# Kernel tuning notes

Measured on AMD Instinct MI355X. Metric: run time of the kernel, lower is better.

The kernel has to match this reference:

```python
import jax, jax.numpy as jnp
import numpy as np

OBS_LEN = 8
PRED_LEN = 12
BATCH = 65536
EMB = 64
H = 64


def setup_inputs() -> dict:
    key = jax.random.key(0)
    ks = jax.random.split(key, 18)
    s = 1.0 / np.sqrt(H)  # torch default uniform bound scale, used as std here

    def p(k, shape):
        return (jax.random.normal(k, shape, dtype=jnp.float32) * s).astype(jnp.float32)

    return {
        "obs_traj": jax.random.normal(ks[0], (OBS_LEN, BATCH, 2), dtype=jnp.float32),
        "obs_traj_rel": jax.random.normal(ks[1], (OBS_LEN, BATCH, 2), dtype=jnp.float32),
        # encoder params
        "enc_emb_w": p(ks[2], (EMB, 2)),
        "enc_emb_b": p(ks[3], (EMB,)),
        "enc_w_ih": p(ks[4], (4 * H, EMB)),
        "enc_w_hh": p(ks[5], (4 * H, H)),
        "enc_b_ih": p(ks[6], (4 * H,)),
        "enc_b_hh": p(ks[7], (4 * H,)),
        # decoder params
        "dec_emb_w": p(ks[8], (EMB, 2)),
        "dec_emb_b": p(ks[9], (EMB,)),
        "dec_w_ih": p(ks[10], (4 * H, EMB)),
        "dec_w_hh": p(ks[11], (4 * H, H)),
        "dec_b_ih": p(ks[12], (4 * H,)),
        "dec_b_hh": p(ks[13], (4 * H,)),
        "h2p_w": p(ks[14], (2, H)),
        "h2p_b": p(ks[15], (2,)),
    }


def _lstm_cell(h, c, x, w_ih, w_hh, b_ih, b_hh):
    # torch nn.LSTM gate order: i, f, g, o
    gates = x @ w_ih.T + h @ w_hh.T + (b_ih + b_hh)
    i, f, g, o = jnp.split(gates, 4, axis=-1)
    c_new = jax.nn.sigmoid(f) * c + jax.nn.sigmoid(i) * jnp.tanh(g)
    h_new = jax.nn.sigmoid(o) * jnp.tanh(c_new)
    return h_new, c_new


def reference(obs_traj, obs_traj_rel,
              enc_emb_w, enc_emb_b, enc_w_ih, enc_w_hh, enc_b_ih, enc_b_hh,
              dec_emb_w, dec_emb_b, dec_w_ih, dec_w_hh, dec_b_ih, dec_b_hh,
              h2p_w, h2p_b):
    batch = obs_traj_rel.shape[1]

    # ---------- Encoder ----------
    enc_in = obs_traj_rel @ enc_emb_w.T + enc_emb_b  # [T, B, EMB]

    def enc_step(carry, x_t):
        h, c = carry
        h, c = _lstm_cell(h, c, x_t, enc_w_ih, enc_w_hh, enc_b_ih, enc_b_hh)
        return (h, c), None

    h0 = jnp.zeros((batch, H), dtype=obs_traj_rel.dtype)
    c0 = jnp.zeros((batch, H), dtype=obs_traj_rel.dtype)
    (h_enc, _), _ = jax.lax.scan(enc_step, (h0, c0), enc_in)

    # ---------- Decoder ----------
    dec_h = h_enc                                   # final encoder hidden seeds decoder
    dec_c = jnp.zeros((batch, H), dtype=obs_traj_rel.dtype)
    last_pos_rel = obs_traj_rel[-1]
    dec_in = last_pos_rel @ dec_emb_w.T + dec_emb_b  # [B, EMB]

    def dec_step(carry, _):
        h, c, x = carry
        h, c = _lstm_cell(h, c, x, dec_w_ih, dec_w_hh, dec_b_ih, dec_b_hh)
        rel_pos = h @ h2p_w.T + h2p_b               # [B, 2]
        x_next = rel_pos @ dec_emb_w.T + dec_emb_b  # [B, EMB]
        return (h, c, x_next), rel_pos

    (_, _, _), pred_traj_fake_rel = jax.lax.scan(
        dec_step, (dec_h, dec_c, dec_in), None, length=PRED_LEN)
    return pred_traj_fake_rel  # [PRED_LEN, B, 2]
```

## Files before the change

kernel.cpp:

```cpp
#include <hip/hip_runtime.h>

#define OBS_LEN 8
#define PRED_LEN 12
#define TILE_B 64
#define NTHREADS 256
#define HSTR 72

typedef __attribute__((ext_vector_type(8))) short short8;
typedef __attribute__((ext_vector_type(4))) float floatx4;
typedef __attribute__((ext_vector_type(2))) float floatx2;
typedef __attribute__((ext_vector_type(4))) unsigned short ushortx4;
typedef unsigned short u16;
typedef unsigned int u32;

__device__ __forceinline__ u16 f2bf(float f) {
  __bf16 b = (__bf16)f;
  return __builtin_bit_cast(u16, b);
}
__device__ __forceinline__ float bf2f(u16 h) {
  return __builtin_bit_cast(float, ((u32)h) << 16);
}
__device__ __forceinline__ float rndbf(float f) { return (float)(__bf16)f; }

#if __has_builtin(__builtin_amdgcn_exp2f)
__device__ __forceinline__ float fexp2_(float x) { return __builtin_amdgcn_exp2f(x); }
#else
__device__ __forceinline__ float fexp2_(float x) { return exp2f(x); }
#endif
#if __has_builtin(__builtin_amdgcn_rcpf)
__device__ __forceinline__ float rcp_nr(float x) {
  float r = __builtin_amdgcn_rcpf(x);
  return r * (2.0f - x * r);
}
#else
__device__ __forceinline__ float rcp_nr(float x) { return 1.0f / x; }
#endif

#define L2E 1.442695040888963f

__device__ __forceinline__ floatx4 mfma_bf(short8 a, short8 b, floatx4 c) {
  return __builtin_amdgcn_mfma_f32_16x16x32_bf16(a, b, c, 0, 0, 0);
}

__device__ __forceinline__ void load_afrags(const float* __restrict__ W,
                                            short8 (&af)[4][2],
                                            int u0, int q, int l16) {
#pragma unroll
  for (int t = 0; t < 4; ++t)
#pragma unroll
    for (int kf = 0; kf < 2; ++kf) {
      const float* src = W + (t * 64 + u0 + l16) * 64 + kf * 32 + q * 8;
      const floatx4 w0 = *(const floatx4*)src;
      const floatx4 w1 = *(const floatx4*)(src + 4);
      short8 a;
#pragma unroll
      for (int j = 0; j < 4; ++j) {
        a[j] = (short)f2bf(w0[j]);
        a[j + 4] = (short)f2bf(w1[j]);
      }
      af[t][kf] = a;
    }
}

__device__ __forceinline__ void bstep_h(const u16* __restrict__ rdh,
                                        const short8 (&afh)[4][2],
                                        const float (&bv)[4][4],
                                        floatx4 (&acc)[4][4], int q, int l16) {
#pragma unroll
  for (int n = 0; n < 4; ++n)
#pragma unroll
    for (int t = 0; t < 4; ++t)
#pragma unroll
      for (int r = 0; r < 4; ++r) acc[n][t][r] = bv[t][r];
#pragma unroll
  for (int n = 0; n < 4; ++n) {
    const int s = n * 16 + l16;
    const short8 hb0 = *(const short8*)(rdh + s * HSTR + q * 8);
    const short8 hb1 = *(const short8*)(rdh + s * HSTR + 32 + q * 8);
#pragma unroll
    for (int t = 0; t < 4; ++t) {
      acc[n][t] = mfma_bf(afh[t][0], hb0, acc[n][t]);
      acc[n][t] = mfma_bf(afh[t][1], hb1, acc[n][t]);
    }
  }
}

__device__ __forceinline__ void bstep_x(const u16* __restrict__ rdx,
                                        u16* __restrict__ wrh,
                                        const short8 (&afx)[4][2],
                                        floatx4 (&acc)[4][4], float (&c)[4][4],
                                        int q, int l16, int u0) {
#pragma unroll
  for (int n = 0; n < 4; ++n) {
    const int s = n * 16 + l16;
    const short8 xb0 = *(const short8*)(rdx + s * HSTR + q * 8);
    const short8 xb1 = *(const short8*)(rdx + s * HSTR + 32 + q * 8);
#pragma unroll
    for (int t = 0; t < 4; ++t) {
      acc[n][t] = mfma_bf(afx[t][0], xb0, acc[n][t]);
      acc[n][t] = mfma_bf(afx[t][1], xb1, acc[n][t]);
    }
  }
#pragma unroll
  for (int n = 0; n < 4; ++n) {
    const int s = n * 16 + l16;
    ushortx4 o;
#pragma unroll
    for (int r = 0; r < 4; ++r) {
      const float ig = acc[n][0][r], fg = acc[n][1][r];
      const float gg = acc[n][2][r], og = acc[n][3][r];
      const float ei = fexp2_(ig * -L2E);
      const float ef = fexp2_(fg * -L2E);
      const float eg = fexp2_(gg * (2.0f * L2E));
      const float eo = fexp2_(og * -L2E);
      const float A = 1.0f + ei;
      const float Bg = eg + 1.0f;
      const float F = 1.0f + ef;
      const float P = A * Bg;
      const float cc = (c[n][r] * P + (eg - 1.0f) * F) * rcp_nr(F * P);
      c[n][r] = cc;
      const float ec = fexp2_(cc * (2.0f * L2E));
      const float h = (ec - 1.0f) * rcp_nr((1.0f + eo) * (ec + 1.0f));
      o[r] = f2bf(h);
    }
    *(ushortx4*)(wrh + s * HSTR + u0 + q * 4) = o;
  }
}

__device__ __forceinline__ void axphase(const float* __restrict__ orow,
                                        const float* __restrict__ ew0,
                                        const float* __restrict__ ew1,
                                        const float* __restrict__ eb,
                                        u16* __restrict__ xw, int s, int p) {
  const floatx2 rr = *(const floatx2*)(orow + s * 2);
  const float r0 = rndbf(rr.x);
  const float r1 = rndbf(rr.y);
#pragma unroll
  for (int i4 = 0; i4 < 4; ++i4) {
    ushortx4 v;
#pragma unroll
    for (int ii = 0; ii < 4; ++ii) {
      const int e = p * 16 + i4 * 4 + ii;
      const float xe = r0 * ew0[e] + r1 * ew1[e] + eb[e];
      v[ii] = f2bf(xe);
    }
    *(ushortx4*)(xw + s * HSTR + p * 16 + i4 * 4) = v;
  }
}

__device__ __forceinline__ void areldot(const u16* __restrict__ h,
                                        const float* __restrict__ hw0,
                                        const float* __restrict__ hw1,
                                        float b2p0, float b2p1, int s, int p,
                                        float& r0, float& r1) {
  float d0 = 0.f, d1 = 0.f;
#pragma unroll
  for (int i4 = 0; i4 < 4; ++i4) {
    const ushortx4 hv4 = *(const ushortx4*)(h + s * HSTR + p * 16 + i4 * 4);
#pragma unroll
    for (int ii = 0; ii < 4; ++ii) {
      const int u = p * 16 + i4 * 4 + ii;
      const float hv = bf2f(hv4[ii]);
      d0 += hv * hw0[u];
      d1 += hv * hw1[u];
    }
  }
  d0 += __shfl_xor(d0, 1);
  d0 += __shfl_xor(d0, 2);
  d1 += __shfl_xor(d1, 1);
  d1 += __shfl_xor(d1, 2);
  r0 = d0 + b2p0;
  r1 = d1 + b2p1;
}

__global__ void __launch_bounds__(NTHREADS, 2)
lstm_kernel(const float* __restrict__ obs_rel,
            const float* __restrict__ enc_emb_w, const float* __restrict__ enc_emb_b,
            const float* __restrict__ enc_w_ih, const float* __restrict__ enc_w_hh,
            const float* __restrict__ enc_b_ih, const float* __restrict__ enc_b_hh,
            const float* __restrict__ dec_emb_w, const float* __restrict__ dec_emb_b,
            const float* __restrict__ dec_w_ih, const float* __restrict__ dec_w_hh,
            const float* __restrict__ dec_b_ih, const float* __restrict__ dec_b_hh,
            const float* __restrict__ h2p_w, const float* __restrict__ h2p_b,
            float* __restrict__ out, int batch) {
  __shared__ __align__(16) u16 hS[2][TILE_B * HSTR];
  __shared__ __align__(16) u16 xS[2][TILE_B * HSTR];
  __shared__ float ew0e[64], ew1e[64], ebe[64];
  __shared__ float ew0d[64], ew1d[64], ebd[64];
  __shared__ float hw0[64], hw1[64];

  const int tid = threadIdx.x;
  const int wv = tid >> 6, lane = tid & 63;
  const int q = lane >> 4, l16 = lane & 15;
  const int u0 = wv << 4;
  const int s4 = tid >> 2, p4 = tid & 3;
  const long S0 = (long)blockIdx.x * TILE_B;

  if (tid < 64) {
    ew0e[tid] = rndbf(enc_emb_w[tid * 2]);
    ew1e[tid] = rndbf(enc_emb_w[tid * 2 + 1]);
    ebe[tid] = enc_emb_b[tid];
    ew0d[tid] = rndbf(dec_emb_w[tid * 2]);
    ew1d[tid] = rndbf(dec_emb_w[tid * 2 + 1]);
    ebd[tid] = dec_emb_b[tid];
    hw0[tid] = rndbf(h2p_w[tid]);
    hw1[tid] = rndbf(h2p_w[64 + tid]);
  }
  for (int i = tid; i < TILE_B * HSTR / 2; i += NTHREADS) ((u32*)&hS[0][0])[i] = 0;

  short8 afh[4][2], afx[4][2];
  floatx4 acc[4][4];
  float bv[4][4], c[4][4];
  load_afrags(enc_w_hh, afh, u0, q, l16);
  load_afrags(enc_w_ih, afx, u0, q, l16);
#pragma unroll
  for (int t = 0; t < 4; ++t)
#pragma unroll
    for (int r = 0; r < 4; ++r) {
      const int g = t * 64 + u0 + q * 4 + r;
      bv[t][r] = enc_b_ih[g] + enc_b_hh[g];
      c[t][r] = 0.f;
    }
  const float b2p0 = h2p_b[0], b2p1 = h2p_b[1];
  __syncthreads();
  axphase(obs_rel + S0 * 2, ew0e, ew1e, ebe, xS[0], s4, p4);
  __syncthreads();

  int pb = 0;
#pragma unroll 1
  for (int t = 0; t < OBS_LEN; ++t) {
    const int tn = t + 1;
    const float* orow = obs_rel + (long)((tn < 8) ? tn : 7) * batch * 2 + S0 * 2;
    if (tn < 8)
      axphase(orow, ew0e, ew1e, ebe, xS[tn & 1], s4, p4);
    else
      axphase(orow, ew0d, ew1d, ebd, xS[0], s4, p4);
    bstep_h(hS[pb], afh, bv, acc, q, l16);
    bstep_x(xS[t & 1], hS[pb ^ 1], afx, acc, c, q, l16, u0);
    __syncthreads();
    pb ^= 1;
  }

  load_afrags(dec_w_hh, afh, u0, q, l16);
  load_afrags(dec_w_ih, afx, u0, q, l16);
#pragma unroll
  for (int t = 0; t < 4; ++t)
#pragma unroll
    for (int r = 0; r < 4; ++r) {
      const int g = t * 64 + u0 + q * 4 + r;
      bv[t][r] = dec_b_ih[g] + dec_b_hh[g];
      c[t][r] = 0.f;
    }
  bstep_h(hS[pb], afh, bv, acc, q, l16);
  bstep_x(xS[0], hS[pb ^ 1], afx, acc, c, q, l16, u0);
  __syncthreads();
  pb ^= 1;

#pragma unroll 1
  for (int j = 1; j < PRED_LEN; ++j) {
    float r0, r1;
    areldot(hS[pb], hw0, hw1, b2p0, b2p1, s4, p4, r0, r1);
    if (p4 == 0)
      *(floatx2*)(out + (long)(j - 1) * batch * 2 + (S0 + s4) * 2) = floatx2{r0, r1};
    {
      const float rb0 = rndbf(r0), rb1 = rndbf(r1);
#pragma unroll
      for (int i4 = 0; i4 < 4; ++i4) {
        ushortx4 v;
#pragma unroll
        for (int ii = 0; ii < 4; ++ii) {
          const int e = p4 * 16 + i4 * 4 + ii;
          const float xe = rb0 * ew0d[e] + rb1 * ew1d[e] + ebd[e];
          v[ii] = f2bf(xe);
        }
        *(ushortx4*)(&xS[0][0] + s4 * HSTR + p4 * 16 + i4 * 4) = v;
      }
    }
    bstep_h(hS[pb], afh, bv, acc, q, l16);
    __syncthreads();
    bstep_x(xS[0], hS[pb ^ 1], afx, acc, c, q, l16, u0);
    __syncthreads();
    pb ^= 1;
  }

  {
    float r0, r1;
    areldot(hS[pb], hw0, hw1, b2p0, b2p1, s4, p4, r0, r1);
    if (p4 == 0)
      *(floatx2*)(out + (long)(PRED_LEN - 1) * batch * 2 + (S0 + s4) * 2) =
          floatx2{r0, r1};
  }
}

extern "C" void kernel_launch(void* const* d_in, const int* in_sizes, int n_in,
                              void* d_out, int out_size, void* d_ws, size_t ws_size,
                              hipStream_t stream) {
  const float* obs_rel = (const float*)d_in[1];
  const int batch = in_sizes[1] / (OBS_LEN * 2);

  const int blocks = batch / TILE_B;
  hipLaunchKernelGGL(lstm_kernel, dim3(blocks), dim3(NTHREADS), 0, stream,
                     obs_rel,
                     (const float*)d_in[2], (const float*)d_in[3],
                     (const float*)d_in[4], (const float*)d_in[5],
                     (const float*)d_in[6], (const float*)d_in[7],
                     (const float*)d_in[8], (const float*)d_in[9],
                     (const float*)d_in[10], (const float*)d_in[11],
                     (const float*)d_in[12], (const float*)d_in[13],
                     (const float*)d_in[14], (const float*)d_in[15],
                     (float*)d_out, batch);
}
```

Measured before the change: 240.5 us.

## Fuse LSTM h/x GEMMs per batch slice to cut accumulators and raise occupancy

Merges the separate hidden and input MFMA passes into one cell step that processes each 16-row batch slice fully, so only 4 accumulators are live instead of 16. The gate math and embedding generation are rewritten with float2 vectors so the compiler can use packed FP32 ops. Launch bounds go from 2 to 3 blocks per SIMD-set. The decoder's h-MFMA no longer overlaps the barrier after the x write, which loses some latency hiding, and the tighter register budget risks spills.

```diff
diff --git a/kernel.cpp b/kernel.cpp
--- a/kernel.cpp
+++ b/kernel.cpp
@@ -10,8 +10,11 @@
 typedef __attribute__((ext_vector_type(4))) float floatx4;
 typedef __attribute__((ext_vector_type(2))) float floatx2;
 typedef __attribute__((ext_vector_type(4))) unsigned short ushortx4;
+typedef __attribute__((ext_vector_type(2))) unsigned int u32x2;
 typedef unsigned short u16;
 typedef unsigned int u32;
+
+#define L2E 1.442695040888963f
 
 __device__ __forceinline__ u16 f2bf(float f) {
   __bf16 b = (__bf16)f;
@@ -27,16 +30,24 @@
 #else
 __device__ __forceinline__ float fexp2_(float x) { return exp2f(x); }
 #endif
+__device__ __forceinline__ floatx2 exp2v(floatx2 x) {
+  floatx2 r;
+  r.x = fexp2_(x.x);
+  r.y = fexp2_(x.y);
+  return r;
+}
 #if __has_builtin(__builtin_amdgcn_rcpf)
-__device__ __forceinline__ float rcp_nr(float x) {
-  float r = __builtin_amdgcn_rcpf(x);
+__device__ __forceinline__ floatx2 rcp2(floatx2 x) {
+  floatx2 r;
+  r.x = __builtin_amdgcn_rcpf(x.x);
+  r.y = __builtin_amdgcn_rcpf(x.y);
   return r * (2.0f - x * r);
 }
 #else
-__device__ __forceinline__ float rcp_nr(float x) { return 1.0f / x; }
+__device__ __forceinline__ floatx2 rcp2(floatx2 x) {
+  return floatx2{1.0f / x.x, 1.0f / x.y};
+}
 #endif
-
-#define L2E 1.442695040888963f
 
 __device__ __forceinline__ floatx4 mfma_bf(short8 a, short8 b, floatx4 c) {
   return __builtin_amdgcn_mfma_f32_16x16x32_bf16(a, b, c, 0, 0, 0);
@@ -62,118 +73,101 @@
     }
 }
 
-__device__ __forceinline__ void bstep_h(const u16* __restrict__ rdh,
-                                        const short8 (&afh)[4][2],
-                                        const float (&bv)[4][4],
-                                        floatx4 (&acc)[4][4], int q, int l16) {
-#pragma unroll
-  for (int n = 0; n < 4; ++n)
-#pragma unroll
-    for (int t = 0; t < 4; ++t)
-#pragma unroll
-      for (int r = 0; r < 4; ++r) acc[n][t][r] = bv[t][r];
+__device__ __forceinline__ void cell_step(const u16* __restrict__ rdh,
+                                          const u16* __restrict__ rdx,
+                                          u16* __restrict__ wrh,
+                                          const short8 (&afh)[4][2],
+                                          const short8 (&afx)[4][2],
+                                          const floatx4 (&bacc)[4],
+                                          floatx2 (&c)[4][2],
+                                          int q, int l16, int u0) {
 #pragma unroll
   for (int n = 0; n < 4; ++n) {
     const int s = n * 16 + l16;
     const short8 hb0 = *(const short8*)(rdh + s * HSTR + q * 8);
     const short8 hb1 = *(const short8*)(rdh + s * HSTR + 32 + q * 8);
-#pragma unroll
-    for (int t = 0; t < 4; ++t) {
-      acc[n][t] = mfma_bf(afh[t][0], hb0, acc[n][t]);
-      acc[n][t] = mfma_bf(afh[t][1], hb1, acc[n][t]);
-    }
-  }
-}
-
-__device__ __forceinline__ void bstep_x(const u16* __restrict__ rdx,
-                                        u16* __restrict__ wrh,
-                                        const short8 (&afx)[4][2],
-                                        floatx4 (&acc)[4][4], float (&c)[4][4],
-                                        int q, int l16, int u0) {
-#pragma unroll
-  for (int n = 0; n < 4; ++n) {
-    const int s = n * 16 + l16;
     const short8 xb0 = *(const short8*)(rdx + s * HSTR + q * 8);
     const short8 xb1 = *(const short8*)(rdx + s * HSTR + 32 + q * 8);
-#pragma unroll
-    for (int t = 0; t < 4; ++t) {
-      acc[n][t] = mfma_bf(afx[t][0], xb0, acc[n][t]);
-      acc[n][t] = mfma_bf(afx[t][1], xb1, acc[n][t]);
-    }
-  }
-#pragma unroll
-  for (int n = 0; n < 4; ++n) {
-    const int s = n * 16 + l16;
-    ushortx4 o;
-#pragma unroll
-    for (int r = 0; r < 4; ++r) {
-      const float ig = acc[n][0][r], fg = acc[n][1][r];
-      const float gg = acc[n][2][r], og = acc[n][3][r];
-      const float ei = fexp2_(ig * -L2E);
-      const float ef = fexp2_(fg * -L2E);
-      const float eg = fexp2_(gg * (2.0f * L2E));
-      const float eo = fexp2_(og * -L2E);
-      const float A = 1.0f + ei;
-      const float Bg = eg + 1.0f;
-      const float F = 1.0f + ef;
-      const float P = A * Bg;
-      const float cc = (c[n][r] * P + (eg - 1.0f) * F) * rcp_nr(F * P);
-      c[n][r] = cc;
-      const float ec = fexp2_(cc * (2.0f * L2E));
-      const float h = (ec - 1.0f) * rcp_nr((1.0f + eo) * (ec + 1.0f));
-      o[r] = f2bf(h);
-    }
-    *(ushortx4*)(wrh + s * HSTR + u0 + q * 4) = o;
-  }
-}
-
-__device__ __forceinline__ void axphase(const float* __restrict__ orow,
-                                        const float* __restrict__ ew0,
-                                        const float* __restrict__ ew1,
-                                        const float* __restrict__ eb,
-                                        u16* __restrict__ xw, int s, int p) {
-  const floatx2 rr = *(const floatx2*)(orow + s * 2);
-  const float r0 = rndbf(rr.x);
-  const float r1 = rndbf(rr.y);
+    floatx4 acc[4];
+#pragma unroll
+    for (int t = 0; t < 4; ++t) acc[t] = mfma_bf(afh[t][0], hb0, bacc[t]);
+#pragma unroll
+    for (int t = 0; t < 4; ++t) acc[t] = mfma_bf(afx[t][0], xb0, acc[t]);
+#pragma unroll
+    for (int t = 0; t < 4; ++t) acc[t] = mfma_bf(afh[t][1], hb1, acc[t]);
+#pragma unroll
+    for (int t = 0; t < 4; ++t) acc[t] = mfma_bf(afx[t][1], xb1, acc[t]);
+    u32 hpk[2];
+#pragma unroll
+    for (int p = 0; p < 2; ++p) {
+      const floatx2 iv = {acc[0][2 * p], acc[0][2 * p + 1]};
+      const floatx2 fv = {acc[1][2 * p], acc[1][2 * p + 1]};
+      const floatx2 gv = {acc[2][2 * p], acc[2][2 * p + 1]};
+      const floatx2 ov = {acc[3][2 * p], acc[3][2 * p + 1]};
+      const floatx2 ei = exp2v(iv * -L2E);
+      const floatx2 ef = exp2v(fv * -L2E);
+      const floatx2 eg = exp2v(gv * (2.0f * L2E));
+      const floatx2 eo = exp2v(ov * -L2E);
+      const floatx2 A = ei + 1.0f;
+      const floatx2 F = ef + 1.0f;
+      const floatx2 Bg = eg + 1.0f;
+      const floatx2 P = A * Bg;
+      const floatx2 num = c[n][p] * P + (eg - 1.0f) * F;
+      const floatx2 cn = num * rcp2(F * P);
+      c[n][p] = cn;
+      const floatx2 ec = exp2v(cn * (2.0f * L2E));
+      const floatx2 h = (ec - 1.0f) * rcp2((eo + 1.0f) * (ec + 1.0f));
+      hpk[p] = (u32)f2bf(h.x) | ((u32)f2bf(h.y) << 16);
+    }
+    *(u32x2*)(wrh + s * HSTR + u0 + q * 4) = u32x2{hpk[0], hpk[1]};
+  }
+}
+
+__device__ __forceinline__ void xgen16(float rb0, float rb1,
+                                       const float* __restrict__ ew0,
+                                       const float* __restrict__ ew1,
+                                       const float* __restrict__ eb,
+                                       u16* __restrict__ xw, int s, int p) {
 #pragma unroll
   for (int i4 = 0; i4 < 4; ++i4) {
-    ushortx4 v;
-#pragma unroll
-    for (int ii = 0; ii < 4; ++ii) {
-      const int e = p * 16 + i4 * 4 + ii;
-      const float xe = r0 * ew0[e] + r1 * ew1[e] + eb[e];
-      v[ii] = f2bf(xe);
-    }
-    *(ushortx4*)(xw + s * HSTR + p * 16 + i4 * 4) = v;
+    const int e = p * 16 + i4 * 4;
+    const floatx2 wa0 = *(const floatx2*)(ew0 + e);
+    const floatx2 wa1 = *(const floatx2*)(ew0 + e + 2);
+    const floatx2 wb0 = *(const floatx2*)(ew1 + e);
+    const floatx2 wb1 = *(const floatx2*)(ew1 + e + 2);
+    const floatx2 ba0 = *(const floatx2*)(eb + e);
+    const floatx2 ba1 = *(const floatx2*)(eb + e + 2);
+    const floatx2 x0 = wa0 * rb0 + (wb0 * rb1 + ba0);
+    const floatx2 x1 = wa1 * rb0 + (wb1 * rb1 + ba1);
+    const u32x2 pk = {(u32)f2bf(x0.x) | ((u32)f2bf(x0.y) << 16),
+                      (u32)f2bf(x1.x) | ((u32)f2bf(x1.y) << 16)};
+    *(u32x2*)(xw + s * HSTR + e) = pk;
   }
 }
 
 __device__ __forceinline__ void areldot(const u16* __restrict__ h,
-                                        const float* __restrict__ hw0,
-                                        const float* __restrict__ hw1,
+                                        const floatx2* __restrict__ hwp,
                                         float b2p0, float b2p1, int s, int p,
                                         float& r0, float& r1) {
-  float d0 = 0.f, d1 = 0.f;
+  floatx2 d = {0.f, 0.f};
 #pragma unroll
   for (int i4 = 0; i4 < 4; ++i4) {
     const ushortx4 hv4 = *(const ushortx4*)(h + s * HSTR + p * 16 + i4 * 4);
 #pragma unroll
     for (int ii = 0; ii < 4; ++ii) {
       const int u = p * 16 + i4 * 4 + ii;
-      const float hv = bf2f(hv4[ii]);
-      d0 += hv * hw0[u];
-      d1 += hv * hw1[u];
-    }
-  }
-  d0 += __shfl_xor(d0, 1);
-  d0 += __shfl_xor(d0, 2);
-  d1 += __shfl_xor(d1, 1);
-  d1 += __shfl_xor(d1, 2);
-  r0 = d0 + b2p0;
-  r1 = d1 + b2p1;
-}
-
-__global__ void __launch_bounds__(NTHREADS, 2)
+      d = hwp[u] * bf2f(hv4[ii]) + d;
+    }
+  }
+  d.x += __shfl_xor(d.x, 1);
+  d.x += __shfl_xor(d.x, 2);
+  d.y += __shfl_xor(d.y, 1);
+  d.y += __shfl_xor(d.y, 2);
+  r0 = d.x + b2p0;
+  r1 = d.y + b2p1;
+}
+
+__global__ void __launch_bounds__(NTHREADS, 3)
 lstm_kernel(const float* __restrict__ obs_rel,
             const float* __restrict__ enc_emb_w, const float* __restrict__ enc_emb_b,
             const float* __restrict__ enc_w_ih, const float* __restrict__ enc_w_hh,
@@ -187,7 +181,7 @@
   __shared__ __align__(16) u16 xS[2][TILE_B * HSTR];
   __shared__ float ew0e[64], ew1e[64], ebe[64];
   __shared__ float ew0d[64], ew1d[64], ebd[64];
-  __shared__ float hw0[64], hw1[64];
+  __shared__ __align__(8) floatx2 hwp[64];
 
   const int tid = threadIdx.x;
   const int wv = tid >> 6, lane = tid & 63;
@@ -203,27 +197,31 @@
     ew0d[tid] = rndbf(dec_emb_w[tid * 2]);
     ew1d[tid] = rndbf(dec_emb_w[tid * 2 + 1]);
     ebd[tid] = dec_emb_b[tid];
-    hw0[tid] = rndbf(h2p_w[tid]);
-    hw1[tid] = rndbf(h2p_w[64 + tid]);
+    hwp[tid] = floatx2{rndbf(h2p_w[tid]), rndbf(h2p_w[64 + tid])};
   }
   for (int i = tid; i < TILE_B * HSTR / 2; i += NTHREADS) ((u32*)&hS[0][0])[i] = 0;
 
   short8 afh[4][2], afx[4][2];
-  floatx4 acc[4][4];
-  float bv[4][4], c[4][4];
+  floatx4 bacc[4];
+  floatx2 c[4][2];
   load_afrags(enc_w_hh, afh, u0, q, l16);
   load_afrags(enc_w_ih, afx, u0, q, l16);
 #pragma unroll
-  for (int t = 0; t < 4; ++t)
+  for (int t = 0; t < 4; ++t) {
 #pragma unroll
     for (int r = 0; r < 4; ++r) {
       const int g = t * 64 + u0 + q * 4 + r;
-      bv[t][r] = enc_b_ih[g] + enc_b_hh[g];
-      c[t][r] = 0.f;
-    }
+      bacc[t][r] = enc_b_ih[g] + enc_b_hh[g];
+    }
+  }
+#pragma unroll
+  for (int n = 0; n < 4; ++n) c[n][0] = c[n][1] = floatx2{0.f, 0.f};
   const float b2p0 = h2p_b[0], b2p1 = h2p_b[1];
   __syncthreads();
-  axphase(obs_rel + S0 * 2, ew0e, ew1e, ebe, xS[0], s4, p4);
+  {
+    const floatx2 rr = *(const floatx2*)(obs_rel + (S0 + s4) * 2);
+    xgen16(rndbf(rr.x), rndbf(rr.y), ew0e, ew1e, ebe, xS[0], s4, p4);
+  }
   __syncthreads();
 
   int pb = 0;
@@ -231,12 +229,12 @@
   for (int t = 0; t < OBS_LEN; ++t) {
     const int tn = t + 1;
     const float* orow = obs_rel + (long)((tn < 8) ? tn : 7) * batch * 2 + S0 * 2;
+    const floatx2 rr = *(const floatx2*)(orow + s4 * 2);
     if (tn < 8)
-      axphase(orow, ew0e, ew1e, ebe, xS[tn & 1], s4, p4);
+      xgen16(rndbf(rr.x), rndbf(rr.y), ew0e, ew1e, ebe, xS[tn & 1], s4, p4);
     else
-      axphase(orow, ew0d, ew1d, ebd, xS[0], s4, p4);
-    bstep_h(hS[pb], afh, bv, acc, q, l16);
-    bstep_x(xS[t & 1], hS[pb ^ 1], afx, acc, c, q, l16, u0);
+      xgen16(rndbf(rr.x), rndbf(rr.y), ew0d, ew1d, ebd, xS[0], s4, p4);
+    cell_step(hS[pb], xS[t & 1], hS[pb ^ 1], afh, afx, bacc, c, q, l16, u0);
     __syncthreads();
     pb ^= 1;
   }
@@ -244,48 +242,35 @@
   load_afrags(dec_w_hh, afh, u0, q, l16);
   load_afrags(dec_w_ih, afx, u0, q, l16);
 #pragma unroll
-  for (int t = 0; t < 4; ++t)
+  for (int t = 0; t < 4; ++t) {
 #pragma unroll
     for (int r = 0; r < 4; ++r) {
       const int g = t * 64 + u0 + q * 4 + r;
-      bv[t][r] = dec_b_ih[g] + dec_b_hh[g];
-      c[t][r] = 0.f;
-    }
-  bstep_h(hS[pb], afh, bv, acc, q, l16);
-  bstep_x(xS[0], hS[pb ^ 1], afx, acc, c, q, l16, u0);
+      bacc[t][r] = dec_b_ih[g] + dec_b_hh[g];
+    }
+  }
+#pragma unroll
+  for (int n = 0; n < 4; ++n) c[n][0] = c[n][1] = floatx2{0.f, 0.f};
+  cell_step(hS[pb], xS[0], hS[pb ^ 1], afh, afx, bacc, c, q, l16, u0);
   __syncthreads();
   pb ^= 1;
 
 #pragma unroll 1
   for (int j = 1; j < PRED_LEN; ++j) {
     float r0, r1;
-    areldot(hS[pb], hw0, hw1, b2p0, b2p1, s4, p4, r0, r1);
+    areldot(hS[pb], hwp, b2p0, b2p1, s4, p4, r0, r1);
     if (p4 == 0)
       *(floatx2*)(out + (long)(j - 1) * batch * 2 + (S0 + s4) * 2) = floatx2{r0, r1};
-    {
-      const float rb0 = rndbf(r0), rb1 = rndbf(r1);
-#pragma unroll
-      for (int i4 = 0; i4 < 4; ++i4) {
-        ushortx4 v;
-#pragma unroll
-        for (int ii = 0; ii < 4; ++ii) {
-          const int e = p4 * 16 + i4 * 4 + ii;
-          const float xe = rb0 * ew0d[e] + rb1 * ew1d[e] + ebd[e];
-          v[ii] = f2bf(xe);
-        }
-        *(ushortx4*)(&xS[0][0] + s4 * HSTR + p4 * 16 + i4 * 4) = v;
-      }
-    }
-    bstep_h(hS[pb], afh, bv, acc, q, l16);
+    xgen16(rndbf(r0), rndbf(r1), ew0d, ew1d, ebd, xS[0], s4, p4);
     __syncthreads();
-    bstep_x(xS[0], hS[pb ^ 1], afx, acc, c, q, l16, u0);
+    cell_step(hS[pb], xS[0], hS[pb ^ 1], afh, afx, bacc, c, q, l16, u0);
     __syncthreads();
     pb ^= 1;
   }
 
   {
     float r0, r1;
-    areldot(hS[pb], hw0, hw1, b2p0, b2p1, s4, p4, r0, r1);
+    areldot(hS[pb], hwp, b2p0, b2p1, s4, p4, r0, r1);
     if (p4 == 0)
       *(floatx2*)(out + (long)(PRED_LEN - 1) * batch * 2 + (S0 + s4) * 2) =
           floatx2{r0, r1};
```

Measured after the change: 240.7 us. No clear change (+0.1%).
